# Kernel tuning notes

Measured on AMD Instinct MI355X. Metric: run time of the kernel, lower is better.

Reference implementation:

```python
import jax, jax.numpy as jnp
import numpy as np
from jax import lax

B, A, H, W = 64, 8, 64, 128
T_EXP = 32
ACTION_HORIZON = 64
DS = 1.0          # reward_cfg['ds']
TEMPERATURE = 0.1 # policy_kwargs['temperature'], method='sharpen'
FOV_HALF_ANGLE_DEG = 35.0
FOV_MAX_RANGE = 100


def _build_buffers():
    # per-action 3x3 one-hot transition kernels: weight 1.0 at 'center' cell,
    # 0.0 at left/right cells (as in MaxEntIRL.__init__ with policy_method='pp')
    center = [[2, 2], [2, 1], [2, 0], [1, 2], [1, 0], [0, 2], [0, 1], [0, 0]]
    tp = np.zeros((A, 1, 3, 3), np.float32)
    for i, (r, c) in enumerate(center):
        tp[i, 0, r, c] = 1.0
    # trapezoidal FOV mask built on a (2H, W) grid, then cropped to first H rows
    rows = np.arange(2 * H, dtype=np.float32)[:, None]
    cols = np.arange(W, dtype=np.float32)[None, :]
    half = np.tan(np.deg2rad(FOV_HALF_ANGLE_DEG)) * rows
    mask = ((np.abs(cols - (W - 1) / 2.0) <= half) & (rows <= FOV_MAX_RANGE))
    fov = mask.astype(np.float32)[:H][None, None]  # (1,1,H,W)
    dyn = np.array([[-1, -1], [-1, 0], [-1, 1], [0, -1],
                    [0, 1], [1, -1], [1, 0], [1, 1]], np.int32)
    return jnp.asarray(tp), jnp.asarray(fov), jnp.asarray(dyn)


def setup_inputs() -> dict:
    key = jax.random.key(0)
    k1, k2 = jax.random.split(key)
    policy = jax.random.normal(k1, (B, A, H, W), jnp.float32)
    # expert SE(2)-like poses; only [:, :, :2, 2] translations are read.
    # Scale to [0,100) so grid cells spread over the map before clamping.
    expert = jax.random.uniform(k2, (B, T_EXP, 3, 3), jnp.float32) * 100.0
    tp, fov, dyn = _build_buffers()
    return {"policy": policy, "expert": expert, "transition_probs": tp,
            "fov_mask": fov, "dynamics": dyn, "action_horizon": ACTION_HORIZON}


def reference(policy, expert, transition_probs, fov_mask, dynamics, action_horizon):
    Bn, An, Hn, Wn = policy.shape
    n_states = Hn * Wn
    barange = jnp.arange(Bn)

    # expert poses -> clamped grid cells  (S: (B, T, 2))
    S = jnp.floor_divide(expert[:, :, :2, 2], DS).astype(jnp.int32)
    S = jnp.stack([jnp.clip(S[..., 0], 0, Hn - 1),
                   jnp.clip(S[..., 1], 0, Wn - 1)], axis=-1)

    # earliest pose inside FOV (argmax of bool gives first True, else 0)
    mask2d = fov_mask[0, 0]
    in_fov = mask2d[S[..., 0], S[..., 1]] > 0  # (B, T)
    idx0 = jnp.argmax(in_fov, axis=1)
    S0c = S[barange, idx0]     # (B, 2) start cell
    S1c = S[:, -1]             # (B, 2) terminal cell
    S0 = S0c[:, 0] * Wn + S0c[:, 1]
    S1 = S1c[:, 0] * Wn + S1c[:, 1]

    # sharpen policy over action dim (stable softmax with temperature)
    logits = (policy - jnp.max(policy, axis=1, keepdims=True)) / TEMPERATURE
    policy_2d = jax.nn.softmax(logits, axis=1)  # (B, A, H, W)

    mu0 = jnp.zeros((Bn, n_states), jnp.float32).at[barange, S0].set(1.0)

    def step(carry, _):
        prev, total = carry
        # zero_terminal_state: kill visitation mass at the terminal cell
        prev_z = prev.at[barange, S1].set(0.0)
        pm = policy_2d * prev_z.reshape(Bn, 1, Hn, Wn)  # (B, A, H, W)
        new = lax.conv_general_dilated(
            pm, transition_probs, window_strides=(1, 1),
            padding=[(1, 1), (1, 1)],
            dimension_numbers=("NCHW", "OIHW", "NCHW"),
            feature_group_count=An)
        new = jnp.sum(new, axis=1).reshape(Bn, n_states)
        return (new, total + prev_z), None

    (last, total), _ = lax.scan(step, (mu0, jnp.zeros_like(mu0)),
                                None, length=action_horizon - 1)
    mu = (total + last).reshape(Bn, Hn, Wn)

    # greedy rollout (torch runs this under no_grad)
    policy_flat = policy.reshape(Bn, An, n_states)
    most_likely_action = jnp.argmax(policy_flat, axis=1)  # (B, n_states)
    most_likely_action = lax.stop_gradient(most_likely_action)

    def roll(St, _):
        a = most_likely_action[barange, St]
        coord = jnp.stack([St // Wn, St % Wn], axis=1) + dynamics[a]
        coord = jnp.stack([jnp.clip(coord[:, 0], 0, Hn - 1),
                           jnp.clip(coord[:, 1], 0, Wn - 1)], axis=1)
        return coord[:, 0] * Wn + coord[:, 1], coord

    _, coords = lax.scan(roll, S0, None, length=action_horizon - 1)  # (T-1,B,2)
    states = jnp.concatenate([S0c[None].astype(coords.dtype), coords],
                             axis=0).transpose(1, 0, 2)  # (B, T, 2)
    bidx = jnp.broadcast_to(barange[:, None], (Bn, action_horizon))
    states_grid = jnp.zeros((Bn, Hn, Wn), jnp.float32).at[
        bidx, states[..., 0], states[..., 1]].add(1.0)
    return mu, states_grid, states
```

## Files before the change

### kernel.cpp

```cpp
#include <hip/hip_runtime.h>

#define THREADS 512

typedef unsigned int u32;

constexpr int BN = 64, AN = 8, HN = 64, WN = 128;
constexpr int HWN = HN * WN;
constexpr int TEXP = 32, AH = 64;
constexpr int PSTR = 136, PROWS = 66;
constexpr int PGUARD = 8;
constexpr int PBUF = PGUARD + PROWS * PSTR;
constexpr size_t LDS_BYTES = (size_t)AN * HWN * 2;

constexpr int GYc[8] = { 1, 1, 1, 0, 0, -1, -1, -1 };
constexpr int GXc[8] = { 1, 0, -1, 1, -1, 1, 0, -1 };

typedef _Float16 h2 __attribute__((ext_vector_type(2)));

union V4 { uint4 q; u32 u[4]; h2 p[4]; _Float16 h[8]; };

__device__ __forceinline__ u32 ab16(u32 hi, u32 lo) {
    return (u32)((((unsigned long long)hi << 32) | lo) >> 16);
}

__device__ __forceinline__ void shiftLR(const V4& d, u32 eLhi, u32 eRlo, V4& L, V4& R) {
    u32 m1 = ab16(d.u[1], d.u[0]);
    u32 m2 = ab16(d.u[2], d.u[1]);
    u32 m3 = ab16(d.u[3], d.u[2]);
    L.u[0] = ab16(d.u[0], eLhi); L.u[1] = m1; L.u[2] = m2; L.u[3] = m3;
    R.u[0] = m1; R.u[1] = m2; R.u[2] = m3; R.u[3] = ab16(eRlo, d.u[3]);
}

__device__ __forceinline__ u32 dpp_from_left(u32 x) {
    return (u32)__builtin_amdgcn_update_dpp(0, (int)x, 0x111 , 0xf, 0xf, true);
}
__device__ __forceinline__ u32 dpp_from_right(u32 x) {
    return (u32)__builtin_amdgcn_update_dpp(0, (int)x, 0x101 , 0xf, 0xf, true);
}

extern "C" __global__ __launch_bounds__(THREADS, 2)
void maxent_fused(const float* __restrict__ policy,
                  const float* __restrict__ expert,
                  const float* __restrict__ fovm,
                  const int*   __restrict__ dyn,
                  float* __restrict__ out)
{
    (void)dyn;
    extern __shared__ char smem[];
    const int tid  = threadIdx.x;
    const int lane = tid & 63;
    const bool isScan = blockIdx.x < BN;
    const int b = isScan ? (int)blockIdx.x : (int)blockIdx.x - BN;

    int Sr = 0, Sc = 0; bool infov = false;
    if (lane < TEXP) {
        float e0 = expert[b * (TEXP * 9) + lane * 9 + 2];
        float e1 = expert[b * (TEXP * 9) + lane * 9 + 5];
        int r = (int)floorf(e0); r = r < 0 ? 0 : (r > HN - 1 ? HN - 1 : r);
        int c = (int)floorf(e1); c = c < 0 ? 0 : (c > WN - 1 ? WN - 1 : c);
        Sr = r; Sc = c;
        infov = fovm[r * WN + c] > 0.0f;
    }
    unsigned long long fmask = __ballot(infov);
    int idx0 = fmask ? (__ffsll(fmask) - 1) : 0;
    const int S0r = __shfl(Sr, idx0), S0c = __shfl(Sc, idx0);
    const int S1r = __shfl(Sr, TEXP - 1), S1c = __shfl(Sc, TEXP - 1);
    const bool S0eqS1 = (S0r == S1r) && (S0c == S1c);

    if (isScan) {
        _Float16* Pl = (_Float16*)smem;

        const float* pb = policy + (size_t)b * AN * HWN;
        #pragma unroll
        for (int kk = 0; kk < 4; ++kk) {
            const int pix = (kk * THREADS + tid) * 4;
            float v[8][4];
            float m[4] = {-3.4e38f, -3.4e38f, -3.4e38f, -3.4e38f};
            #pragma unroll
            for (int a = 0; a < 8; ++a) {
                float4 f = *(const float4*)(pb + a * HWN + pix);
                v[a][0] = f.x; v[a][1] = f.y; v[a][2] = f.z; v[a][3] = f.w;
                m[0] = fmaxf(m[0], f.x); m[1] = fmaxf(m[1], f.y);
                m[2] = fmaxf(m[2], f.z); m[3] = fmaxf(m[3], f.w);
            }
            float s[4] = {0.f, 0.f, 0.f, 0.f};
            #pragma unroll
            for (int a = 0; a < 8; ++a)
                #pragma unroll
                for (int j = 0; j < 4; ++j) { v[a][j] = __expf((v[a][j] - m[j]) * 10.0f); s[j] += v[a][j]; }
            float inv[4];
            #pragma unroll
            for (int j = 0; j < 4; ++j) inv[j] = 1.0f / s[j];
            #pragma unroll
            for (int a = 0; a < 8; ++a) {
                u32 lo = (u32)__builtin_bit_cast(unsigned short, (_Float16)(v[a][0] * inv[0]))
                       | ((u32)__builtin_bit_cast(unsigned short, (_Float16)(v[a][1] * inv[1])) << 16);
                u32 hi = (u32)__builtin_bit_cast(unsigned short, (_Float16)(v[a][2] * inv[2]))
                       | ((u32)__builtin_bit_cast(unsigned short, (_Float16)(v[a][3] * inv[3])) << 16);
                uint2 pk2; pk2.x = lo; pk2.y = hi;
                *(uint2*)(Pl + a * HWN + pix) = pk2;
            }
        }
        __syncthreads();

        const int wv = tid >> 6;
        const int y0 = 8 * wv + 2 * (lane >> 4);
        const int x0 = (lane & 15) * 8;

        V4 pa0[8], pa1[8];
        #pragma unroll
        for (int a = 0; a < 8; ++a) {
            const int gy = GYc[a], gx = GXc[a];
            #pragma unroll
            for (int r = 0; r < 2; ++r) {
                const int ny = y0 + r + gy;
                V4 wvv;
                #pragma unroll
                for (int k = 0; k < 8; ++k) wvv.h[k] = (_Float16)0.0f;
                if (ny >= 0 && ny < HN) {
                    const _Float16* base = Pl + a * HWN + ny * WN + x0;
                    V4 qq; qq.q = *(const uint4*)base;
                    if (gx == 0) {
                        wvv = qq;
                    } else if (gx == 1) {
                        _Float16 e = (x0 < WN - 8) ? base[8] : base[7];
                        #pragma unroll
                        for (int k = 0; k < 7; ++k) wvv.h[k] = qq.h[k + 1];
                        wvv.h[7] = e;
                    } else {
                        _Float16 e = (x0 > 0) ? base[-1] : base[0];
                        wvv.h[0] = e;
                        #pragma unroll
                        for (int k = 1; k < 8; ++k) wvv.h[k] = qq.h[k - 1];
                    }
                }
                if (r == 0) pa0[a] = wvv; else pa1[a] = wvv;
            }
        }
        __syncthreads();

        _Float16* B0 = (_Float16*)smem;
        _Float16* B1 = B0 + PBUF;
        for (int i = tid; i < 2 * PBUF; i += THREADS) B0[i] = (_Float16)0.0f;
        __syncthreads();
        if (tid == 0 && !S0eqS1) B0[PGUARD + (S0r + 1) * PSTR + S0c] = (_Float16)1.0f;
        __syncthreads();

        const bool own0 = (y0     == S1r) && (S1c >= x0) && (S1c < x0 + 8);
        const bool own1 = (y0 + 1 == S1r) && (S1c >= x0) && (S1c < x0 + 8);
        V4 zA, zB, sA, sB;
        #pragma unroll
        for (int q = 0; q < 4; ++q) {
            u32 mA = ~0u, mB = ~0u;
            if (own0 && ((S1c - x0) >> 1) == q) mA = ((S1c - x0) & 1) ? 0x0000FFFFu : 0xFFFF0000u;
            if (own1 && ((S1c - x0) >> 1) == q) mB = ((S1c - x0) & 1) ? 0x0000FFFFu : 0xFFFF0000u;
            zA.u[q] = mA; zB.u[q] = mB;
            u32 v0 = 0;
            if (!S0eqS1 && y0 == S0r && S0c >= x0 && S0c < x0 + 8 && ((S0c - x0) >> 1) == q)
                v0 = ((S0c - x0) & 1) ? 0x3C000000u : 0x00003C00u;
            u32 v1 = 0;
            if (!S0eqS1 && y0 + 1 == S0r && S0c >= x0 && S0c < x0 + 8 && ((S0c - x0) >> 1) == q)
                v1 = ((S0c - x0) & 1) ? 0x3C000000u : 0x00003C00u;
            sA.u[q] = v0; sB.u[q] = v1;
        }

        float total[16];
        #pragma unroll
        for (int k = 0; k < 16; ++k) total[k] = 0.f;
        V4 nnA, nnB, tA, tB;
        #pragma unroll
        for (int q = 0; q < 4; ++q) { nnA.u[q] = 0; nnB.u[q] = 0; tA.u[q] = 0; tB.u[q] = 0; }

        const int offT  = PGUARD + y0 * PSTR + x0;
        const int offD  = offT + 3 * PSTR;
        const int offW0 = offT + PSTR;
        const int offW1 = offW0 + PSTR;

        #define COMPUTE_OWN(ownA_, ownB_)                                              \
        {                                                                              \
            u32 packL = (sA.u[3] >> 16) | (sB.u[3] & 0xFFFF0000u);                     \
            u32 packR = (sA.u[0] & 0xFFFFu) | (sB.u[0] << 16);                         \
            u32 pL = dpp_from_left(packL);                                             \
            u32 pR = dpp_from_right(packR);                                            \
            V4 AL, AR, BL, BR;                                                         \
            shiftLR(sA, pL << 16,          pR & 0xFFFFu, AL, AR);                      \
            shiftLR(sB, pL & 0xFFFF0000u,  pR >> 16,     BL, BR);                      \
            _Pragma("unroll")                                                          \
            for (int q = 0; q < 4; ++q) {                                              \
                h2 a = pa0[0].p[q] * BR.p[q]; a += pa0[1].p[q] * sB.p[q];              \
                a += pa0[2].p[q] * BL.p[q];   a += pa0[3].p[q] * AR.p[q];              \
                a += pa0[4].p[q] * AL.p[q];                                            \
                h2 bb = pa1[3].p[q] * BR.p[q]; bb += pa1[4].p[q] * BL.p[q];            \
                bb += pa1[5].p[q] * AR.p[q];   bb += pa1[6].p[q] * sA.p[q];            \
                bb += pa1[7].p[q] * AL.p[q];                                           \
                ownA_.p[q] = a; ownB_.p[q] = bb;                                       \
            }                                                                          \
        }

        V4 ownA, ownB;
        COMPUTE_OWN(ownA, ownB)

        _Float16* RB = B0; _Float16* WB = B1;
        for (int it = 0; it < AH - 1; ++it) {
            const bool active = (8 * wv <= S0r + it + 1) && (8 * wv + 7 >= S0r - it - 1);
            if (active) {
                V4 qT, qD;
                qT.q = *(const uint4*)(RB + offT);
                qD.q = *(const uint4*)(RB + offD);

                #pragma unroll
                for (int q = 0; q < 4; ++q) { tA.p[q] += sA.p[q]; tB.p[q] += sB.p[q]; }
                if ((it & 3) == 3 || it == AH - 2) {
                    #pragma unroll
                    for (int q = 0; q < 4; ++q) {
                        total[2*q]       += (float)tA.p[q].x;  total[2*q + 1]     += (float)tA.p[q].y;
                        total[8 + 2*q]   += (float)tB.p[q].x;  total[8 + 2*q + 1] += (float)tB.p[q].y;
                        tA.u[q] = 0; tB.u[q] = 0;
                    }
                }

                u32 packL_TD = (qT.u[3] >> 16) | (qD.u[3] & 0xFFFF0000u);
                u32 packR_TD = (qT.u[0] & 0xFFFFu) | (qD.u[0] << 16);
                u32 pLtd = dpp_from_left(packL_TD);
                u32 pRtd = dpp_from_right(packR_TD);
                V4 TL, TR, DL, DR;
                shiftLR(qT, pLtd << 16,          pRtd & 0xFFFFu, TL, TR);
                shiftLR(qD, pLtd & 0xFFFF0000u,  pRtd >> 16,     DL, DR);
                #pragma unroll
                for (int q = 0; q < 4; ++q) {
                    h2 a = ownA.p[q] + pa0[5].p[q] * TR.p[q];
                    a += pa0[6].p[q] * qT.p[q];  a += pa0[7].p[q] * TL.p[q];
                    h2 bb = ownB.p[q] + pa1[0].p[q] * DR.p[q];
                    bb += pa1[1].p[q] * qD.p[q]; bb += pa1[2].p[q] * DL.p[q];
                    nnA.p[q] = a; nnB.p[q] = bb;
                    sA.u[q] = nnA.u[q] & zA.u[q];
                    sB.u[q] = nnB.u[q] & zB.u[q];
                }
                *(uint4*)(WB + offW0) = sA.q;
                *(uint4*)(WB + offW1) = sB.q;

                COMPUTE_OWN(ownA, ownB)
            }
            __syncthreads();
            _Float16* t = RB; RB = WB; WB = t;
        }
        #undef COMPUTE_OWN

        float* ob0 = out + (size_t)b * HWN + y0 * WN + x0;
        float* ob1 = ob0 + WN;
        #pragma unroll
        for (int k = 0; k < 8; ++k) {
            ob0[k] = total[k]     + (float)nnA.h[k];
            ob1[k] = total[8 + k] + (float)nnB.h[k];
        }

    } else {
        short* amap = (short*)smem;
        float* grid = (float*)(smem + 16384);
        const float* pb = policy + (size_t)b * AN * HWN;
        #pragma unroll
        for (int c = 0; c < 4; ++c) {
            const int pix = (c * THREADS + tid) * 4;
            float4 f0 = *(const float4*)(pb + pix);
            float b0 = f0.x, b1 = f0.y, b2 = f0.z, b3 = f0.w;
            int a0 = 0, a1 = 0, a2 = 0, a3 = 0;
            #pragma unroll
            for (int a = 1; a < 8; ++a) {
                float4 f = *(const float4*)(pb + a * HWN + pix);
                if (f.x > b0) { b0 = f.x; a0 = a; }
                if (f.y > b1) { b1 = f.y; a1 = a; }
                if (f.z > b2) { b2 = f.z; a2 = a; }
                if (f.w > b3) { b3 = f.w; a3 = a; }
            }
            uint2 pk2;
            pk2.x = (u32)a0 | ((u32)a1 << 16);
            pk2.y = (u32)a2 | ((u32)a3 << 16);
            *(uint2*)(amap + pix) = pk2;
        }
        for (int i = tid; i < HWN; i += THREADS) grid[i] = 0.f;
        __syncthreads();

        if (tid == 0) {
            float* so = out + 2 * (size_t)HWN * BN + b * (AH * 2);
            int cr = S0r, cc = S0c;
            so[0] = (float)cr; so[1] = (float)cc;
            grid[cr * WN + cc] += 1.0f;
            for (int t = 1; t < AH; ++t) {
                const int a = amap[cr * WN + cc];
                const int dr = (a < 3) ? -1 : ((a < 5) ? 0 : 1);
                int dc;
                if (a < 3) dc = a - 1;
                else if (a == 3) dc = -1;
                else if (a == 4) dc = 1;
                else dc = a - 6;
                cr += dr; cc += dc;
                cr = cr < 0 ? 0 : (cr > HN - 1 ? HN - 1 : cr);
                cc = cc < 0 ? 0 : (cc > WN - 1 ? WN - 1 : cc);
                so[t * 2] = (float)cr; so[t * 2 + 1] = (float)cc;
                grid[cr * WN + cc] += 1.0f;
            }
        }
        __syncthreads();
        float* sg = out + (size_t)HWN * BN + b * HWN;
        for (int i = tid; i < HWN; i += THREADS) sg[i] = grid[i];
    }
}

extern "C" void kernel_launch(void* const* d_in, const int* in_sizes, int n_in,
                              void* d_out, int out_size, void* d_ws, size_t ws_size,
                              hipStream_t stream) {
    const float* policy = (const float*)d_in[0];
    const float* expert = (const float*)d_in[1];
    const float* fovm   = (const float*)d_in[3];
    const int*   dyn    = (const int*)d_in[4];
    float* out = (float*)d_out;

    (void)hipFuncSetAttribute((const void*)maxent_fused,
                              hipFuncAttributeMaxDynamicSharedMemorySize,
                              (int)LDS_BYTES);
    hipLaunchKernelGGL(maxent_fused, dim3(2 * BN), dim3(THREADS), LDS_BYTES, stream,
                       policy, expert, fovm, dyn, out);
}
```

Before: 52.81 us.

## Pack two batch scans per 1024-thread block sharing LDS

Scan blocks now use 1024 threads, with two 512-thread groups each handling a different batch element. The softmax for the two batches is computed one after the other into the shared LDS, and each group gathers its own neighbour weights into registers before the buffer is reused as two pairs of ping-pong buffers. This halves the number of scan blocks and shares block-wide barriers between two batches. The cost is extra serial softmax passes, more syncthreads, and coupled progress of the two groups. The greedy-rollout blocks also move to 1024 threads.

```diff
diff --git a/kernel.cpp b/kernel.cpp
--- a/kernel.cpp
+++ b/kernel.cpp
@@ -1,12 +1,13 @@
 #include <hip/hip_runtime.h>
 
-#define THREADS 512
+#define THREADS 1024
 
 typedef unsigned int u32;
 
 constexpr int BN = 64, AN = 8, HN = 64, WN = 128;
 constexpr int HWN = HN * WN;
 constexpr int TEXP = 32, AH = 64;
+constexpr int SCANB = 32;
 constexpr int PSTR = 136, PROWS = 66;
 constexpr int PGUARD = 8;
 constexpr int PBUF = PGUARD + PROWS * PSTR;
@@ -38,7 +39,7 @@
     return (u32)__builtin_amdgcn_update_dpp(0, (int)x, 0x101 , 0xf, 0xf, true);
 }
 
-extern "C" __global__ __launch_bounds__(THREADS, 2)
+extern "C" __global__ __launch_bounds__(THREADS, 4)
 void maxent_fused(const float* __restrict__ policy,
                   const float* __restrict__ expert,
                   const float* __restrict__ fovm,
@@ -49,8 +50,11 @@
     extern __shared__ char smem[];
     const int tid  = threadIdx.x;
     const int lane = tid & 63;
-    const bool isScan = blockIdx.x < BN;
-    const int b = isScan ? (int)blockIdx.x : (int)blockIdx.x - BN;
+    const bool isScan = blockIdx.x < SCANB;
+    const int wv16 = tid >> 6;
+    const int grp  = wv16 >> 3;
+    const int lw   = wv16 & 7;
+    const int b = isScan ? ((int)blockIdx.x * 2 + grp) : ((int)blockIdx.x - SCANB);
 
     int Sr = 0, Sc = 0; bool infov = false;
     if (lane < TEXP) {
@@ -70,80 +74,86 @@
     if (isScan) {
         _Float16* Pl = (_Float16*)smem;
 
-        const float* pb = policy + (size_t)b * AN * HWN;
-        #pragma unroll
-        for (int kk = 0; kk < 4; ++kk) {
-            const int pix = (kk * THREADS + tid) * 4;
-            float v[8][4];
-            float m[4] = {-3.4e38f, -3.4e38f, -3.4e38f, -3.4e38f};
+        const int y0 = 8 * lw + 2 * (lane >> 4);
+        const int x0 = (lane & 15) * 8;
+
+        V4 pa0[8], pa1[8];
+
+        for (int g = 0; g < 2; ++g) {
+            const int bb = (int)blockIdx.x * 2 + g;
+            const float* pb = policy + (size_t)bb * AN * HWN;
             #pragma unroll
-            for (int a = 0; a < 8; ++a) {
-                float4 f = *(const float4*)(pb + a * HWN + pix);
-                v[a][0] = f.x; v[a][1] = f.y; v[a][2] = f.z; v[a][3] = f.w;
-                m[0] = fmaxf(m[0], f.x); m[1] = fmaxf(m[1], f.y);
-                m[2] = fmaxf(m[2], f.z); m[3] = fmaxf(m[3], f.w);
-            }
-            float s[4] = {0.f, 0.f, 0.f, 0.f};
-            #pragma unroll
-            for (int a = 0; a < 8; ++a)
-                #pragma unroll
-                for (int j = 0; j < 4; ++j) { v[a][j] = __expf((v[a][j] - m[j]) * 10.0f); s[j] += v[a][j]; }
-            float inv[4];
-            #pragma unroll
-            for (int j = 0; j < 4; ++j) inv[j] = 1.0f / s[j];
-            #pragma unroll
-            for (int a = 0; a < 8; ++a) {
-                u32 lo = (u32)__builtin_bit_cast(unsigned short, (_Float16)(v[a][0] * inv[0]))
-                       | ((u32)__builtin_bit_cast(unsigned short, (_Float16)(v[a][1] * inv[1])) << 16);
-                u32 hi = (u32)__builtin_bit_cast(unsigned short, (_Float16)(v[a][2] * inv[2]))
-                       | ((u32)__builtin_bit_cast(unsigned short, (_Float16)(v[a][3] * inv[3])) << 16);
-                uint2 pk2; pk2.x = lo; pk2.y = hi;
-                *(uint2*)(Pl + a * HWN + pix) = pk2;
-            }
-        }
+            for (int kk = 0; kk < 2; ++kk) {
+                const int pix = (kk * THREADS + tid) * 4;
+                float v[8][4];
+                float m[4] = {-3.4e38f, -3.4e38f, -3.4e38f, -3.4e38f};
+                #pragma unroll
+                for (int a = 0; a < 8; ++a) {
+                    float4 f = *(const float4*)(pb + a * HWN + pix);
+                    v[a][0] = f.x; v[a][1] = f.y; v[a][2] = f.z; v[a][3] = f.w;
+                    m[0] = fmaxf(m[0], f.x); m[1] = fmaxf(m[1], f.y);
+                    m[2] = fmaxf(m[2], f.z); m[3] = fmaxf(m[3], f.w);
+                }
+                float s[4] = {0.f, 0.f, 0.f, 0.f};
+                #pragma unroll
+                for (int a = 0; a < 8; ++a)
+                    #pragma unroll
+                    for (int j = 0; j < 4; ++j) { v[a][j] = __expf((v[a][j] - m[j]) * 10.0f); s[j] += v[a][j]; }
+                float inv[4];
+                #pragma unroll
+                for (int j = 0; j < 4; ++j) inv[j] = 1.0f / s[j];
+                #pragma unroll
+                for (int a = 0; a < 8; ++a) {
+                    u32 lo = (u32)__builtin_bit_cast(unsigned short, (_Float16)(v[a][0] * inv[0]))
+                           | ((u32)__builtin_bit_cast(unsigned short, (_Float16)(v[a][1] * inv[1])) << 16);
+                    u32 hi = (u32)__builtin_bit_cast(unsigned short, (_Float16)(v[a][2] * inv[2]))
+                           | ((u32)__builtin_bit_cast(unsigned short, (_Float16)(v[a][3] * inv[3])) << 16);
+                    uint2 pk2; pk2.x = lo; pk2.y = hi;
+                    *(uint2*)(Pl + a * HWN + pix) = pk2;
+                }
+            }
+            __syncthreads();
+
+            if (grp == g) {
+                #pragma unroll
+                for (int a = 0; a < 8; ++a) {
+                    const int gy = GYc[a], gx = GXc[a];
+                    #pragma unroll
+                    for (int r = 0; r < 2; ++r) {
+                        const int ny = y0 + r + gy;
+                        V4 wvv;
+                        #pragma unroll
+                        for (int k = 0; k < 8; ++k) wvv.h[k] = (_Float16)0.0f;
+                        if (ny >= 0 && ny < HN) {
+                            const _Float16* base = Pl + a * HWN + ny * WN + x0;
+                            V4 qq; qq.q = *(const uint4*)base;
+                            if (gx == 0) {
+                                wvv = qq;
+                            } else if (gx == 1) {
+                                _Float16 e = (x0 < WN - 8) ? base[8] : base[7];
+                                #pragma unroll
+                                for (int k = 0; k < 7; ++k) wvv.h[k] = qq.h[k + 1];
+                                wvv.h[7] = e;
+                            } else {
+                                _Float16 e = (x0 > 0) ? base[-1] : base[0];
+                                wvv.h[0] = e;
+                                #pragma unroll
+                                for (int k = 1; k < 8; ++k) wvv.h[k] = qq.h[k - 1];
+                            }
+                        }
+                        if (r == 0) pa0[a] = wvv; else pa1[a] = wvv;
+                    }
+                }
+            }
+            __syncthreads();
+        }
+
+        _Float16* gbase = (_Float16*)smem + grp * 2 * PBUF;
+        _Float16* B0 = gbase;
+        _Float16* B1 = gbase + PBUF;
+        for (int i = tid; i < 4 * PBUF; i += THREADS) ((_Float16*)smem)[i] = (_Float16)0.0f;
         __syncthreads();
-
-        const int wv = tid >> 6;
-        const int y0 = 8 * wv + 2 * (lane >> 4);
-        const int x0 = (lane & 15) * 8;
-
-        V4 pa0[8], pa1[8];
-        #pragma unroll
-        for (int a = 0; a < 8; ++a) {
-            const int gy = GYc[a], gx = GXc[a];
-            #pragma unroll
-            for (int r = 0; r < 2; ++r) {
-                const int ny = y0 + r + gy;
-                V4 wvv;
-                #pragma unroll
-                for (int k = 0; k < 8; ++k) wvv.h[k] = (_Float16)0.0f;
-                if (ny >= 0 && ny < HN) {
-                    const _Float16* base = Pl + a * HWN + ny * WN + x0;
-                    V4 qq; qq.q = *(const uint4*)base;
-                    if (gx == 0) {
-                        wvv = qq;
-                    } else if (gx == 1) {
-                        _Float16 e = (x0 < WN - 8) ? base[8] : base[7];
-                        #pragma unroll
-                        for (int k = 0; k < 7; ++k) wvv.h[k] = qq.h[k + 1];
-                        wvv.h[7] = e;
-                    } else {
-                        _Float16 e = (x0 > 0) ? base[-1] : base[0];
-                        wvv.h[0] = e;
-                        #pragma unroll
-                        for (int k = 1; k < 8; ++k) wvv.h[k] = qq.h[k - 1];
-                    }
-                }
-                if (r == 0) pa0[a] = wvv; else pa1[a] = wvv;
-            }
-        }
-        __syncthreads();
-
-        _Float16* B0 = (_Float16*)smem;
-        _Float16* B1 = B0 + PBUF;
-        for (int i = tid; i < 2 * PBUF; i += THREADS) B0[i] = (_Float16)0.0f;
-        __syncthreads();
-        if (tid == 0 && !S0eqS1) B0[PGUARD + (S0r + 1) * PSTR + S0c] = (_Float16)1.0f;
+        if ((tid & 511) == 0 && !S0eqS1) B0[PGUARD + (S0r + 1) * PSTR + S0c] = (_Float16)1.0f;
         __syncthreads();
 
         const bool own0 = (y0     == S1r) && (S1c >= x0) && (S1c < x0 + 8);
@@ -202,7 +212,7 @@
 
         _Float16* RB = B0; _Float16* WB = B1;
         for (int it = 0; it < AH - 1; ++it) {
-            const bool active = (8 * wv <= S0r + it + 1) && (8 * wv + 7 >= S0r - it - 1);
+            const bool active = (8 * lw <= S0r + it + 1) && (8 * lw + 7 >= S0r - it - 1);
             if (active) {
                 V4 qT, qD;
                 qT.q = *(const uint4*)(RB + offT);
@@ -259,7 +269,7 @@
         float* grid = (float*)(smem + 16384);
         const float* pb = policy + (size_t)b * AN * HWN;
         #pragma unroll
-        for (int c = 0; c < 4; ++c) {
+        for (int c = 0; c < 2; ++c) {
             const int pix = (c * THREADS + tid) * 4;
             float4 f0 = *(const float4*)(pb + pix);
             float b0 = f0.x, b1 = f0.y, b2 = f0.z, b3 = f0.w;
@@ -318,6 +328,6 @@
     (void)hipFuncSetAttribute((const void*)maxent_fused,
                               hipFuncAttributeMaxDynamicSharedMemorySize,
                               (int)LDS_BYTES);
-    hipLaunchKernelGGL(maxent_fused, dim3(2 * BN), dim3(THREADS), LDS_BYTES, stream,
+    hipLaunchKernelGGL(maxent_fused, dim3(SCANB + BN), dim3(THREADS), LDS_BYTES, stream,
                        policy, expert, fovm, dyn, out);
 }
```

Result: slower. 134.1 us (+153.9%).
